# Kernel tuning notes

Hardware: AMD Instinct MI355X
Metric: run time of the kernel (lower is better)

Reference implementation:

```python
import jax, jax.numpy as jnp
import numpy as np

N_NODES = 50000
N_EDGES = 800000
NDIM_IN = 64
EDIM = 32
HIDDEN = 128
NDIM_OUT = 64


def setup_inputs() -> dict:
    key = jax.random.key(0)
    ks = jax.random.split(key, 12)
    glorot = lambda k, fi, fo: jax.random.normal(k, (fi, fo), jnp.float32) * np.sqrt(2.0 / (fi + fo))
    return {
        "x": jax.random.normal(ks[0], (N_NODES, NDIM_IN), jnp.float32),
        "edge_index": jax.random.randint(ks[1], (2, N_EDGES), 0, N_NODES, jnp.int64),
        "edge_attr": jax.random.normal(ks[2], (N_EDGES, EDIM), jnp.float32),
        # layer 1: SAGELayer(ndim_in=64, edim=32, ndim_out=128)
        "W_msg1": glorot(ks[3], NDIM_IN + EDIM, HIDDEN),
        "b_msg1": jnp.zeros((HIDDEN,), jnp.float32),
        "W_app1": glorot(ks[4], NDIM_IN + HIDDEN, HIDDEN),
        "b_app1": jnp.zeros((HIDDEN,), jnp.float32),
        # layer 2: SAGELayer(ndim_in=128, edim=32, ndim_out=64)
        "W_msg2": glorot(ks[5], HIDDEN + EDIM, NDIM_OUT),
        "b_msg2": jnp.zeros((NDIM_OUT,), jnp.float32),
        "W_app2": glorot(ks[6], HIDDEN + NDIM_OUT, NDIM_OUT),
        "b_app2": jnp.zeros((NDIM_OUT,), jnp.float32),
    }


def _sage_layer(x, src, dst, edge_attr, W_msg, b_msg, W_app, b_app):
    # message: per-edge gather of source features, concat with edge attrs, linear
    msg = jnp.concatenate([x[src], edge_attr], axis=-1) @ W_msg + b_msg  # [E, d_out]
    # mean-scatter aggregate at destination nodes (0 for isolated nodes, as in PyG)
    n = x.shape[0]
    summed = jax.ops.segment_sum(msg, dst, num_segments=n)              # [N, d_out]
    cnt = jax.ops.segment_sum(jnp.ones((src.shape[0], 1), x.dtype), dst, num_segments=n)
    aggr = summed / jnp.maximum(cnt, 1.0)
    # update: concat self features with aggregate, linear, relu
    return jax.nn.relu(jnp.concatenate([x, aggr], axis=-1) @ W_app + b_app)


def reference(x, edge_index, edge_attr,
              W_msg1, b_msg1, W_app1, b_app1,
              W_msg2, b_msg2, W_app2, b_app2):
    src, dst = edge_index[0], edge_index[1]
    h = _sage_layer(x, src, dst, edge_attr, W_msg1, b_msg1, W_app1, b_app1)
    # dropout is identity in eval mode
    h = _sage_layer(h, src, dst, edge_attr, W_msg2, b_msg2, W_app2, b_app2)
    return h
```

## Files before the change

kernel.cpp:

```cpp
#include <hip/hip_runtime.h>

#define SCAN_CHUNK 1024
#define NPB 32

typedef unsigned int   uint32;
typedef unsigned short ushort16;
typedef __attribute__((ext_vector_type(8))) short bf16x8;
typedef __attribute__((ext_vector_type(4))) float f32x4;
#define MFMA16(a,b,c) __builtin_amdgcn_mfma_f32_16x16x32_bf16(a,b,c,0,0,0)

__device__ inline float4 f4_xor_add(float4 v, int mask) {
    v.x += __shfl_xor(v.x, mask);
    v.y += __shfl_xor(v.y, mask);
    v.z += __shfl_xor(v.z, mask);
    v.w += __shfl_xor(v.w, mask);
    return v;
}

__device__ inline uint32 pack_bf16x2(float a, float b) {
    uint32 ua = __float_as_uint(a);
    uint32 ub = __float_as_uint(b);
    ua += 0x7FFFu + ((ua >> 16) & 1u);
    ub += 0x7FFFu + ((ub >> 16) & 1u);
    return (ua >> 16) | (ub & 0xFFFF0000u);
}
__device__ inline ushort16 bf16_1(float a) {
    uint32 u = __float_as_uint(a);
    u += 0x7FFFu + ((u >> 16) & 1u);
    return (ushort16)(u >> 16);
}
__device__ inline float bf_lo(uint32 u) { return __uint_as_float(u << 16); }
__device__ inline float bf_hi(uint32 u) { return __uint_as_float(u & 0xFFFF0000u); }

__global__ void cvt_x_kernel(const float4* __restrict__ xin,
                             uint2* __restrict__ xb, int n4)
{
    int i = blockIdx.x * blockDim.x + threadIdx.x;
    if (i < n4) {
        float4 v = xin[i];
        uint2 o;
        o.x = pack_bf16x2(v.x, v.y);
        o.y = pack_bf16x2(v.z, v.w);
        xb[i] = o;
    }
}

__global__ void hist_kernel(const int* __restrict__ dst, int* __restrict__ deg, int E)
{
    int e = blockIdx.x * blockDim.x + threadIdx.x;
    if (e < E) atomicAdd(&deg[dst[e]], 1);
}

__global__ __launch_bounds__(256) void scanA_kernel(const int* __restrict__ deg,
                                                    int* __restrict__ part, int N)
{
    __shared__ int red[256];
    int b = blockIdx.x, t = threadIdx.x;
    int base = b * SCAN_CHUNK;
    int s = 0;
    for (int i = t; i < SCAN_CHUNK; i += 256) {
        int idx = base + i;
        s += (idx < N) ? deg[idx] : 0;
    }
    red[t] = s;
    __syncthreads();
    for (int o = 128; o > 0; o >>= 1) {
        if (t < o) red[t] += red[t + o];
        __syncthreads();
    }
    if (t == 0) part[b] = red[0];
}

__global__ void scanB_kernel(int* __restrict__ part, int* __restrict__ offN, int NCH)
{
    int lane = threadIdx.x;
    int orig = (lane < NCH) ? part[lane] : 0;
    int v = orig;
    for (int s = 1; s < 64; s <<= 1) {
        int t = __shfl_up(v, s);
        if (lane >= s) v += t;
    }
    if (lane < NCH) part[lane] = v - orig;
    if (lane == NCH - 1) *offN = v;
}

__global__ __launch_bounds__(SCAN_CHUNK) void scanC_kernel(const int* __restrict__ deg,
                                                           const int* __restrict__ part,
                                                           int* __restrict__ off,
                                                           int* __restrict__ cursor, int N)
{
    __shared__ int buf[SCAN_CHUNK];
    int b = blockIdx.x, t = threadIdx.x;
    int idx = b * SCAN_CHUNK + t;
    int v = (idx < N) ? deg[idx] : 0;
    buf[t] = v;
    __syncthreads();
    for (int s = 1; s < SCAN_CHUNK; s <<= 1) {
        int tmp = (t >= s) ? buf[t - s] : 0;
        __syncthreads();
        buf[t] += tmp;
        __syncthreads();
    }
    int excl = buf[t] - v + part[b];
    if (idx < N) { off[idx] = excl; cursor[idx] = excl; }
}

__global__ void fill_kernel(const int* __restrict__ src, const int* __restrict__ dst,
                            int* __restrict__ cursor, int2* __restrict__ elist, int E)
{
    int e = blockIdx.x * blockDim.x + threadIdx.x;
    if (e >= E) return;
    int d = dst[e];
    int p = atomicAdd(&cursor[d], 1);
    elist[p] = make_int2(src[e], e);
}

__global__ __launch_bounds__(128) void compose1_kernel(
    const float* __restrict__ Wmsg1, const float* __restrict__ bmsg1,
    const float* __restrict__ Wapp1, const float* __restrict__ bapp1,
    ushort16* __restrict__ Wc1T, float* __restrict__ b1eff, float* __restrict__ bmW1)
{
    int b = blockIdx.x;
    int j = threadIdx.x;
    if (b < 64) {
        Wc1T[(size_t)j * 160 + b] = bf16_1(Wapp1[b * 128 + j]);
    } else if (b < 160) {
        int ar = b - 64;
        float s = 0.f;
        for (int k = 0; k < 128; k++)
            s = fmaf(Wmsg1[ar * 128 + k], Wapp1[(64 + k) * 128 + j], s);
        Wc1T[(size_t)j * 160 + b] = bf16_1(s);
    } else {
        float s = 0.f;
        for (int k = 0; k < 128; k++)
            s = fmaf(bmsg1[k], Wapp1[(64 + k) * 128 + j], s);
        bmW1[j] = s;
        b1eff[j] = bapp1[j] + s;
    }
}

__global__ __launch_bounds__(64) void compose2_kernel(
    const float* __restrict__ Wmsg2, const float* __restrict__ bmsg2,
    const float* __restrict__ Wapp2, const float* __restrict__ bapp2,
    ushort16* __restrict__ Wc2T, float* __restrict__ b2eff, float* __restrict__ bmW2)
{
    int b = blockIdx.x;
    int j = threadIdx.x;
    if (b < 192) {
        Wc2T[(size_t)j * 224 + b] = bf16_1(Wapp2[b * 64 + j]);
    } else if (b < 224) {
        int ar = 128 + (b - 192);
        float s = 0.f;
        for (int k = 0; k < 64; k++)
            s = fmaf(Wmsg2[ar * 64 + k], Wapp2[(128 + k) * 64 + j], s);
        Wc2T[(size_t)j * 224 + b] = bf16_1(s);
    } else {
        float s = 0.f;
        for (int k = 0; k < 64; k++)
            s = fmaf(bmsg2[k], Wapp2[(128 + k) * 64 + j], s);
        bmW2[j] = s;
        b2eff[j] = bapp2[j] + s;
    }
}

__global__ __launch_bounds__(64) void composem_kernel(
    const float* __restrict__ Wmsg2, ushort16* __restrict__ Wm2hT)
{
    int k = blockIdx.x;
    int c = threadIdx.x;
    Wm2hT[(size_t)c * 128 + k] = bf16_1(Wmsg2[k * 64 + c]);
}

__global__ __launch_bounds__(256) void agg1_kernel(const uint4* __restrict__ xb,
                                                   const float4* __restrict__ ea4,
                                                   const int2* __restrict__ elist,
                                                   const int* __restrict__ off,
                                                   float4* __restrict__ A1x,
                                                   float4* __restrict__ A1e, int N)
{
    int wv = (blockIdx.x * blockDim.x + threadIdx.x) >> 6;
    int lane = threadIdx.x & 63;
    if (wv >= N) return;
    int beg = off[wv], end = off[wv + 1];
    float inv = 1.0f / fmaxf((float)(end - beg), 1.0f);

    int g8 = lane >> 3, s8 = lane & 7;

    float ax[8];
#pragma unroll
    for (int q = 0; q < 8; q++) ax[q] = 0.f;
    for (int i = beg + g8; i < end; i += 8) {
        int row = elist[i].x;
        uint4 v = xb[(size_t)row * 8 + s8];
        ax[0] += bf_lo(v.x); ax[1] += bf_hi(v.x);
        ax[2] += bf_lo(v.y); ax[3] += bf_hi(v.y);
        ax[4] += bf_lo(v.z); ax[5] += bf_hi(v.z);
        ax[6] += bf_lo(v.w); ax[7] += bf_hi(v.w);
    }
#pragma unroll
    for (int m = 8; m <= 32; m <<= 1) {
#pragma unroll
        for (int q = 0; q < 8; q++) ax[q] += __shfl_xor(ax[q], m);
    }
    if (lane < 8) {
        float4 o0 = make_float4(ax[0] * inv, ax[1] * inv, ax[2] * inv, ax[3] * inv);
        float4 o1 = make_float4(ax[4] * inv, ax[5] * inv, ax[6] * inv, ax[7] * inv);
        A1x[(size_t)wv * 16 + s8 * 2 + 0] = o0;
        A1x[(size_t)wv * 16 + s8 * 2 + 1] = o1;
    }

    float4 ae = make_float4(0.f, 0.f, 0.f, 0.f);
    for (int i = beg + g8; i < end; i += 8) {
        int eid = elist[i].y;
        float4 v = ea4[(size_t)eid * 8 + s8];
        ae.x += v.x; ae.y += v.y; ae.z += v.z; ae.w += v.w;
    }
    ae = f4_xor_add(ae, 8);
    ae = f4_xor_add(ae, 16);
    ae = f4_xor_add(ae, 32);
    if (lane < 8) {
        ae.x *= inv; ae.y *= inv; ae.z *= inv; ae.w *= inv;
        A1e[(size_t)wv * 8 + s8] = ae;
    }
}

__global__ __launch_bounds__(256) void agg2_kernel(const uint4* __restrict__ g2b,
                                                   const int2* __restrict__ elist,
                                                   const int* __restrict__ off,
                                                   float4* __restrict__ A2g, int N)
{
    int wv = (blockIdx.x * blockDim.x + threadIdx.x) >> 6;
    int lane = threadIdx.x & 63;
    if (wv >= N) return;
    int beg = off[wv], end = off[wv + 1];
    float inv = 1.0f / fmaxf((float)(end - beg), 1.0f);

    int g8 = lane >> 3, s8 = lane & 7;
    float ag[8];
#pragma unroll
    for (int q = 0; q < 8; q++) ag[q] = 0.f;
    for (int i = beg + g8; i < end; i += 8) {
        int row = elist[i].x;
        uint4 v = g2b[(size_t)row * 8 + s8];
        ag[0] += bf_lo(v.x); ag[1] += bf_hi(v.x);
        ag[2] += bf_lo(v.y); ag[3] += bf_hi(v.y);
        ag[4] += bf_lo(v.z); ag[5] += bf_hi(v.z);
        ag[6] += bf_lo(v.w); ag[7] += bf_hi(v.w);
    }
#pragma unroll
    for (int m = 8; m <= 32; m <<= 1) {
#pragma unroll
        for (int q = 0; q < 8; q++) ag[q] += __shfl_xor(ag[q], m);
    }
    if (lane < 8) {
        float4 o0 = make_float4(ag[0] * inv, ag[1] * inv, ag[2] * inv, ag[3] * inv);
        float4 o1 = make_float4(ag[4] * inv, ag[5] * inv, ag[6] * inv, ag[7] * inv);
        A2g[(size_t)wv * 16 + s8 * 2 + 0] = o0;
        A2g[(size_t)wv * 16 + s8 * 2 + 1] = o1;
    }
}

__global__ __launch_bounds__(512) void node1_kernel(
    const uint32* __restrict__ xb,
    const float* __restrict__ A1x,
    const float* __restrict__ A1e,
    const int*   __restrict__ deg,
    const ushort16* __restrict__ Wc1T,
    const float* __restrict__ b1eff,
    const float* __restrict__ bmW1,
    const ushort16* __restrict__ Wm2hT,
    uint32* __restrict__ h1b,
    uint32* __restrict__ g2b,
    int N)
{
    __shared__ ushort16 sFb[NPB][168];
    __shared__ ushort16 sHb[NPB][168];
    __shared__ float sCnt[NPB];

    int t = threadIdx.x;
    int base = blockIdx.x * NPB;
    int tr = t >> 4, c16 = t & 15;
    int v = base + tr;
    bool vok = v < N;

    uint32* sFrow = (uint32*)&sFb[tr][0];
#pragma unroll
    for (int m = 0; m < 5; m++) {
        int d = c16 + 16 * m;
        uint32 w = 0;
        if (vok) {
            if (d < 32) {
                w = xb[(size_t)v * 32 + d];
            } else if (d < 64) {
                int o = (d - 32) * 2;
                w = pack_bf16x2(A1x[(size_t)v * 64 + o], A1x[(size_t)v * 64 + o + 1]);
            } else {
                int o = (d - 64) * 2;
                w = pack_bf16x2(A1e[(size_t)v * 32 + o], A1e[(size_t)v * 32 + o + 1]);
            }
        }
        sFrow[d] = w;
    }
    if (t < NPB) sCnt[t] = (base + t < N) ? (float)deg[base + t] : 1.f;
    __syncthreads();

    int lane = t & 63;
    int wv = t >> 6;
    int lr = lane & 15;
    int kg = lane >> 4;

    f32x4 acc0 = {0.f, 0.f, 0.f, 0.f};
    f32x4 acc1 = {0.f, 0.f, 0.f, 0.f};
    const ushort16* bp1 = &Wc1T[(size_t)(wv * 16 + lr) * 160 + kg * 8];
#pragma unroll
    for (int kt = 0; kt < 5; kt++) {
        bf16x8 a0 = *(const bf16x8*)&sFb[lr][kt * 32 + kg * 8];
        bf16x8 a1 = *(const bf16x8*)&sFb[16 + lr][kt * 32 + kg * 8];
        bf16x8 b  = *(const bf16x8*)&bp1[kt * 32];
        acc0 = MFMA16(a0, b, acc0);
        acc1 = MFMA16(a1, b, acc1);
    }
    int col = wv * 16 + lr;
    float bj = b1eff[col], bw = bmW1[col];
#pragma unroll
    for (int rt = 0; rt < 2; rt++) {
        f32x4 acc = rt ? acc1 : acc0;
        int r0 = rt * 16 + kg * 4;
#pragma unroll
        for (int reg = 0; reg < 4; reg++) {
            float c = sCnt[r0 + reg];
            float hv = fmaxf(acc[reg] + (c > 0.f ? bj : bj - bw), 0.f);
            float other = __shfl_xor(hv, 1);
            if (!(lane & 1))
                ((uint32*)&sHb[r0 + reg][0])[col >> 1] = pack_bf16x2(hv, other);
        }
    }
    __syncthreads();

#pragma unroll
    for (int m = 0; m < 4; m++) {
        int d = c16 + 16 * m;
        if (vok) h1b[(size_t)v * 64 + d] = ((uint32*)&sHb[tr][0])[d];
    }

    int rt2 = wv >> 2, ct2 = wv & 3;
    f32x4 accg = {0.f, 0.f, 0.f, 0.f};
    const ushort16* bp2 = &Wm2hT[(size_t)(ct2 * 16 + lr) * 128 + kg * 8];
#pragma unroll
    for (int kt = 0; kt < 4; kt++) {
        bf16x8 a = *(const bf16x8*)&sHb[rt2 * 16 + lr][kt * 32 + kg * 8];
        bf16x8 b = *(const bf16x8*)&bp2[kt * 32];
        accg = MFMA16(a, b, accg);
    }
    int colg = ct2 * 16 + lr;
    int rg0 = rt2 * 16 + kg * 4;
#pragma unroll
    for (int reg = 0; reg < 4; reg++) {
        float other = __shfl_xor(accg[reg], 1);
        int vr = base + rg0 + reg;
        if (!(lane & 1) && vr < N)
            g2b[(size_t)vr * 32 + (colg >> 1)] = pack_bf16x2(accg[reg], other);
    }
}

__global__ __launch_bounds__(512) void node2_kernel(
    const uint32* __restrict__ h1b,
    const float* __restrict__ A2g,
    const float* __restrict__ A1e,
    const int*   __restrict__ deg,
    const ushort16* __restrict__ Wc2T,
    const float* __restrict__ b2eff,
    const float* __restrict__ bmW2,
    float* __restrict__ out,
    int N)
{
    __shared__ ushort16 sFb[NPB][232];
    __shared__ float sCnt[NPB];

    int t = threadIdx.x;
    int base = blockIdx.x * NPB;
    int tr = t >> 4, c16 = t & 15;
    int v = base + tr;
    bool vok = v < N;

    uint32* sFrow = (uint32*)&sFb[tr][0];
#pragma unroll
    for (int m = 0; m < 7; m++) {
        int d = c16 + 16 * m;
        uint32 w = 0;
        if (vok) {
            if (d < 64) {
                w = h1b[(size_t)v * 64 + d];
            } else if (d < 96) {
                int o = (d - 64) * 2;
                w = pack_bf16x2(A2g[(size_t)v * 64 + o], A2g[(size_t)v * 64 + o + 1]);
            } else {
                int o = (d - 96) * 2;
                w = pack_bf16x2(A1e[(size_t)v * 32 + o], A1e[(size_t)v * 32 + o + 1]);
            }
        }
        sFrow[d] = w;
    }
    if (t < NPB) sCnt[t] = (base + t < N) ? (float)deg[base + t] : 1.f;
    __syncthreads();

    int lane = t & 63;
    int wv = t >> 6;
    int lr = lane & 15;
    int kg = lane >> 4;
    int rt = wv >> 2, ct = wv & 3;

    f32x4 acc = {0.f, 0.f, 0.f, 0.f};
    const ushort16* bp = &Wc2T[(size_t)(ct * 16 + lr) * 224 + kg * 8];
#pragma unroll
    for (int kt = 0; kt < 7; kt++) {
        bf16x8 a = *(const bf16x8*)&sFb[rt * 16 + lr][kt * 32 + kg * 8];
        bf16x8 b = *(const bf16x8*)&bp[kt * 32];
        acc = MFMA16(a, b, acc);
    }
    int col = ct * 16 + lr;
    float bj = b2eff[col], bw = bmW2[col];
    int r0 = rt * 16 + kg * 4;
#pragma unroll
    for (int reg = 0; reg < 4; reg++) {
        int vr = base + r0 + reg;
        float c = sCnt[r0 + reg];
        float bias = (c > 0.f) ? bj : bj - bw;
        if (vr < N) out[(size_t)vr * 64 + col] = fmaxf(acc[reg] + bias, 0.f);
    }
}

extern "C" void kernel_launch(void* const* d_in, const int* in_sizes, int n_in,
                              void* d_out, int out_size, void* d_ws, size_t ws_size,
                              hipStream_t stream) {
    const float* x      = (const float*)d_in[0];
    const int*   ei     = (const int*)d_in[1];
    const float* ea     = (const float*)d_in[2];
    const float* Wmsg1  = (const float*)d_in[3];
    const float* bmsg1  = (const float*)d_in[4];
    const float* Wapp1  = (const float*)d_in[5];
    const float* bapp1  = (const float*)d_in[6];
    const float* Wmsg2  = (const float*)d_in[7];
    const float* bmsg2  = (const float*)d_in[8];
    const float* Wapp2  = (const float*)d_in[9];
    const float* bapp2  = (const float*)d_in[10];

    const int N = in_sizes[0] / 64;
    const int E = in_sizes[1] / 2;
    const int NCH = (N + SCAN_CHUNK - 1) / SCAN_CHUNK;
    const int* src = ei;
    const int* dst = ei + E;

    uint8_t* p = (uint8_t*)d_ws;
    auto alloc = [&](size_t bytes) -> void* {
        void* r = (void*)p;
        p += (bytes + 255) & ~(size_t)255;
        return r;
    };
    int*     deg    = (int*)alloc((size_t)N * 4);
    int*     off    = (int*)alloc((size_t)(N + 1) * 4);
    int*     cursor = (int*)alloc((size_t)N * 4);
    int*     part   = (int*)alloc((size_t)NCH * 4);
    int2*    elist  = (int2*)alloc((size_t)E * 8);
    float*   A1x    = (float*)alloc((size_t)N * 64 * 4);
    float*   A1e    = (float*)alloc((size_t)N * 32 * 4);
    uint32*  xb     = (uint32*)alloc((size_t)N * 32 * 4);
    uint32*  h1b    = (uint32*)alloc((size_t)N * 64 * 4);
    uint32*  g2b    = (uint32*)alloc((size_t)N * 32 * 4);
    ushort16* Wc1T  = (ushort16*)alloc(128 * 160 * 2);
    ushort16* Wc2T  = (ushort16*)alloc(64 * 224 * 2);
    ushort16* Wm2hT = (ushort16*)alloc(64 * 128 * 2);
    float*   b1eff  = (float*)alloc(128 * 4);
    float*   bmW1   = (float*)alloc(128 * 4);
    float*   b2eff  = (float*)alloc(64 * 4);
    float*   bmW2   = (float*)alloc(64 * 4);
    float*   A2g    = A1x;

    hipMemsetAsync(deg, 0, (size_t)N * 4, stream);

    compose1_kernel<<<161, 128, 0, stream>>>(Wmsg1, bmsg1, Wapp1, bapp1,
                                             Wc1T, b1eff, bmW1);
    compose2_kernel<<<225, 64, 0, stream>>>(Wmsg2, bmsg2, Wapp2, bapp2,
                                            Wc2T, b2eff, bmW2);
    composem_kernel<<<128, 64, 0, stream>>>(Wmsg2, Wm2hT);
    {
        int n4 = N * 16;
        cvt_x_kernel<<<(n4 + 255) / 256, 256, 0, stream>>>(
            (const float4*)x, (uint2*)xb, n4);
    }

    hist_kernel<<<(E + 255) / 256, 256, 0, stream>>>(dst, deg, E);
    scanA_kernel<<<NCH, 256, 0, stream>>>(deg, part, N);
    scanB_kernel<<<1, 64, 0, stream>>>(part, off + N, NCH);
    scanC_kernel<<<NCH, SCAN_CHUNK, 0, stream>>>(deg, part, off, cursor, N);
    fill_kernel<<<(E + 255) / 256, 256, 0, stream>>>(src, dst, cursor, elist, E);

    agg1_kernel<<<(N + 3) / 4, 256, 0, stream>>>(
        (const uint4*)xb, (const float4*)ea, elist, off,
        (float4*)A1x, (float4*)A1e, N);
    node1_kernel<<<(N + NPB - 1) / NPB, 512, 0, stream>>>(
        xb, A1x, A1e, deg, Wc1T, b1eff, bmW1, Wm2hT, h1b, g2b, N);

    agg2_kernel<<<(N + 3) / 4, 256, 0, stream>>>(
        (const uint4*)g2b, elist, off, (float4*)A2g, N);
    node2_kernel<<<(N + NPB - 1) / NPB, 512, 0, stream>>>(
        h1b, A2g, A1e, deg, Wc2T, b2eff, bmW2,
        (float*)d_out, N);
}
```

Before: 214.6 us.

## Map eight lanes per node in aggregation kernels, dropping wave-wide shuffle reductions

The CSR gather aggregation kernels now give each node 8 lanes instead of a full 64-lane wave. Each lane loops serially over all incoming edges, and the cross-lane shuffle reduction is removed. In agg1 the x-feature and edge-attribute gathers are fused into one loop, so the edge list is read once. Fewer lanes go idle on low-degree nodes (average degree is about 16), at the cost of less memory-level parallelism per node and more divergence from degree imbalance inside a wave.

```diff
diff --git a/kernel.cpp b/kernel.cpp
--- a/kernel.cpp
+++ b/kernel.cpp
@@ -8,14 +8,6 @@
 typedef __attribute__((ext_vector_type(8))) short bf16x8;
 typedef __attribute__((ext_vector_type(4))) float f32x4;
 #define MFMA16(a,b,c) __builtin_amdgcn_mfma_f32_16x16x32_bf16(a,b,c,0,0,0)
-
-__device__ inline float4 f4_xor_add(float4 v, int mask) {
-    v.x += __shfl_xor(v.x, mask);
-    v.y += __shfl_xor(v.y, mask);
-    v.z += __shfl_xor(v.z, mask);
-    v.w += __shfl_xor(v.w, mask);
-    return v;
-}
 
 __device__ inline uint32 pack_bf16x2(float a, float b) {
     uint32 ua = __float_as_uint(a);
@@ -178,50 +170,34 @@
                                                    float4* __restrict__ A1x,
                                                    float4* __restrict__ A1e, int N)
 {
-    int wv = (blockIdx.x * blockDim.x + threadIdx.x) >> 6;
-    int lane = threadIdx.x & 63;
-    if (wv >= N) return;
-    int beg = off[wv], end = off[wv + 1];
+    int tid = blockIdx.x * blockDim.x + threadIdx.x;
+    int node = tid >> 3;
+    int s8 = tid & 7;
+    if (node >= N) return;
+    int beg = off[node], end = off[node + 1];
     float inv = 1.0f / fmaxf((float)(end - beg), 1.0f);
 
-    int g8 = lane >> 3, s8 = lane & 7;
-
     float ax[8];
 #pragma unroll
     for (int q = 0; q < 8; q++) ax[q] = 0.f;
-    for (int i = beg + g8; i < end; i += 8) {
-        int row = elist[i].x;
-        uint4 v = xb[(size_t)row * 8 + s8];
-        ax[0] += bf_lo(v.x); ax[1] += bf_hi(v.x);
-        ax[2] += bf_lo(v.y); ax[3] += bf_hi(v.y);
-        ax[4] += bf_lo(v.z); ax[5] += bf_hi(v.z);
-        ax[6] += bf_lo(v.w); ax[7] += bf_hi(v.w);
-    }
-#pragma unroll
-    for (int m = 8; m <= 32; m <<= 1) {
-#pragma unroll
-        for (int q = 0; q < 8; q++) ax[q] += __shfl_xor(ax[q], m);
-    }
-    if (lane < 8) {
-        float4 o0 = make_float4(ax[0] * inv, ax[1] * inv, ax[2] * inv, ax[3] * inv);
-        float4 o1 = make_float4(ax[4] * inv, ax[5] * inv, ax[6] * inv, ax[7] * inv);
-        A1x[(size_t)wv * 16 + s8 * 2 + 0] = o0;
-        A1x[(size_t)wv * 16 + s8 * 2 + 1] = o1;
-    }
-
     float4 ae = make_float4(0.f, 0.f, 0.f, 0.f);
-    for (int i = beg + g8; i < end; i += 8) {
-        int eid = elist[i].y;
-        float4 v = ea4[(size_t)eid * 8 + s8];
-        ae.x += v.x; ae.y += v.y; ae.z += v.z; ae.w += v.w;
-    }
-    ae = f4_xor_add(ae, 8);
-    ae = f4_xor_add(ae, 16);
-    ae = f4_xor_add(ae, 32);
-    if (lane < 8) {
-        ae.x *= inv; ae.y *= inv; ae.z *= inv; ae.w *= inv;
-        A1e[(size_t)wv * 8 + s8] = ae;
-    }
+
+    for (int i = beg; i < end; i++) {
+        int2 pr = elist[i];
+        uint4 vx = xb[(size_t)pr.x * 8 + s8];
+        float4 ve = ea4[(size_t)pr.y * 8 + s8];
+        ax[0] += bf_lo(vx.x); ax[1] += bf_hi(vx.x);
+        ax[2] += bf_lo(vx.y); ax[3] += bf_hi(vx.y);
+        ax[4] += bf_lo(vx.z); ax[5] += bf_hi(vx.z);
+        ax[6] += bf_lo(vx.w); ax[7] += bf_hi(vx.w);
+        ae.x += ve.x; ae.y += ve.y; ae.z += ve.z; ae.w += ve.w;
+    }
+    float4 o0 = make_float4(ax[0] * inv, ax[1] * inv, ax[2] * inv, ax[3] * inv);
+    float4 o1 = make_float4(ax[4] * inv, ax[5] * inv, ax[6] * inv, ax[7] * inv);
+    A1x[(size_t)node * 16 + s8 * 2 + 0] = o0;
+    A1x[(size_t)node * 16 + s8 * 2 + 1] = o1;
+    ae.x *= inv; ae.y *= inv; ae.z *= inv; ae.w *= inv;
+    A1e[(size_t)node * 8 + s8] = ae;
 }
 
 __global__ __launch_bounds__(256) void agg2_kernel(const uint4* __restrict__ g2b,
@@ -229,17 +205,18 @@
                                                    const int* __restrict__ off,
                                                    float4* __restrict__ A2g, int N)
 {
-    int wv = (blockIdx.x * blockDim.x + threadIdx.x) >> 6;
-    int lane = threadIdx.x & 63;
-    if (wv >= N) return;
-    int beg = off[wv], end = off[wv + 1];
+    int tid = blockIdx.x * blockDim.x + threadIdx.x;
+    int node = tid >> 3;
+    int s8 = tid & 7;
+    if (node >= N) return;
+    int beg = off[node], end = off[node + 1];
     float inv = 1.0f / fmaxf((float)(end - beg), 1.0f);
 
-    int g8 = lane >> 3, s8 = lane & 7;
     float ag[8];
 #pragma unroll
     for (int q = 0; q < 8; q++) ag[q] = 0.f;
-    for (int i = beg + g8; i < end; i += 8) {
+
+    for (int i = beg; i < end; i++) {
         int row = elist[i].x;
         uint4 v = g2b[(size_t)row * 8 + s8];
         ag[0] += bf_lo(v.x); ag[1] += bf_hi(v.x);
@@ -247,17 +224,10 @@
         ag[4] += bf_lo(v.z); ag[5] += bf_hi(v.z);
         ag[6] += bf_lo(v.w); ag[7] += bf_hi(v.w);
     }
-#pragma unroll
-    for (int m = 8; m <= 32; m <<= 1) {
-#pragma unroll
-        for (int q = 0; q < 8; q++) ag[q] += __shfl_xor(ag[q], m);
-    }
-    if (lane < 8) {
-        float4 o0 = make_float4(ag[0] * inv, ag[1] * inv, ag[2] * inv, ag[3] * inv);
-        float4 o1 = make_float4(ag[4] * inv, ag[5] * inv, ag[6] * inv, ag[7] * inv);
-        A2g[(size_t)wv * 16 + s8 * 2 + 0] = o0;
-        A2g[(size_t)wv * 16 + s8 * 2 + 1] = o1;
-    }
+    float4 o0 = make_float4(ag[0] * inv, ag[1] * inv, ag[2] * inv, ag[3] * inv);
+    float4 o1 = make_float4(ag[4] * inv, ag[5] * inv, ag[6] * inv, ag[7] * inv);
+    A2g[(size_t)node * 16 + s8 * 2 + 0] = o0;
+    A2g[(size_t)node * 16 + s8 * 2 + 1] = o1;
 }
 
 __global__ __launch_bounds__(512) void node1_kernel(
@@ -495,13 +465,13 @@
     scanC_kernel<<<NCH, SCAN_CHUNK, 0, stream>>>(deg, part, off, cursor, N);
     fill_kernel<<<(E + 255) / 256, 256, 0, stream>>>(src, dst, cursor, elist, E);
 
-    agg1_kernel<<<(N + 3) / 4, 256, 0, stream>>>(
+    agg1_kernel<<<(N + 31) / 32, 256, 0, stream>>>(
         (const uint4*)xb, (const float4*)ea, elist, off,
         (float4*)A1x, (float4*)A1e, N);
     node1_kernel<<<(N + NPB - 1) / NPB, 512, 0, stream>>>(
         xb, A1x, A1e, deg, Wc1T, b1eff, bmW1, Wm2hT, h1b, g2b, N);
 
-    agg2_kernel<<<(N + 3) / 4, 256, 0, stream>>>(
+    agg2_kernel<<<(N + 31) / 32, 256, 0, stream>>>(
         (const uint4*)g2b, elist, off, (float4*)A2g, N);
     node2_kernel<<<(N + NPB - 1) / NPB, 512, 0, stream>>>(
         h1b, A2g, A1e, deg, Wc2T, b2eff, bmW2,
```

Measured after the change: 212.2 us. No clear change (-1.1%).
